# Kernel optimization log

Measured on AMD Instinct MI355X. Metric: run time of the kernel, lower is better.

Reference implementation:

```python
import jax, jax.numpy as jnp
import numpy as np

EPS = 1e-12
N_NODES = 100000
N_EDGES = 1600000
IN_CH = 8
N_CLASSES = 16
MAX_ORDER = 1
N_RINGS = 2


def setup_inputs() -> dict:
    key = jax.random.key(0)
    k0, k1, k2, k3, k4 = jax.random.split(key, 5)
    x = jax.random.normal(k0, (N_NODES, IN_CH), dtype=jnp.float32)
    edge_index = jax.random.randint(k1, (2, N_EDGES), 0, N_NODES)
    precomp = jax.random.normal(k2, (N_EDGES, MAX_ORDER + 1, N_RINGS, 2), dtype=jnp.float32)
    connection = jax.random.normal(k3, (N_EDGES, 2), dtype=jnp.float32)
    # n_orders = (prev_order+1)*(max_order+1) with default prev_order=1 -> 2*(max_order+1)
    n_orders = 2 * (MAX_ORDER + 1)
    radial_profile = jax.random.normal(k4, (n_orders, N_RINGS, N_CLASSES, IN_CH), dtype=jnp.float32) * 0.1
    bias = jnp.zeros((N_CLASSES,), dtype=jnp.float32)
    return dict(x=x, edge_index=edge_index, precomp=precomp,
                connection=connection, radial_profile=radial_profile, bias=bias)


def reference(x, edge_index, precomp, connection, radial_profile, bias):
    # x is stacked with zeros -> complex features with a single stream (M=1, input_order=0).
    # Since input_order==0 only, `connection` (parallel transport) is never applied.
    N = x.shape[0]
    O1 = MAX_ORDER + 1
    src = edge_index[0]  # aggregation targets (flow='target_to_source')
    tgt = edge_index[1]  # gathered neighbours (x_j)
    xjr = x[tgt]                      # [E, F] real part
    xji = jnp.zeros_like(xjr)         # [E, F] imaginary part (zeros by construction)
    # m = |output_order - 0| = output_order; sign = np.sign(m) -> 0 for order 0, +1 otherwise
    signs = jnp.sign(jnp.arange(O1, dtype=x.dtype))
    pre_re = jnp.transpose(precomp[..., 0], (0, 2, 1))          # [E, R, O1]
    pre_im = jnp.transpose(precomp[..., 1], (0, 2, 1)) * signs  # [E, R, O1]
    a_re = xjr[:, None, :, None]      # [E, 1, F, 1]
    a_im = xji[:, None, :, None]
    b_re = pre_re[:, :, None, :]      # [E, R, 1, O1]
    b_im = pre_im[:, :, None, :]
    msg_re = a_re * b_re - a_im * b_im   # [E, R, F, O1]
    msg_im = a_re * b_im + a_im * b_re
    aggr_re = jax.ops.segment_sum(msg_re, src, num_segments=N)  # [N, R, F, O1]
    aggr_im = jax.ops.segment_sum(msg_im, src, num_segments=N)
    # update: m_idx = 0*(max_order+1)+output_order, offset=False
    prof = radial_profile[:O1]        # [O1, R, C, F]
    out_re = jnp.einsum('orcf,nrfo->noc', prof, aggr_re)  # [N, O1, C]
    out_im = jnp.einsum('orcf,nrfo->noc', prof, aggr_im)
    mag = jnp.sqrt(jnp.maximum(out_re * out_re + out_im * out_im, EPS))  # [N, O1, C]
    logits = mag.sum(axis=1) + bias   # [N, C]
    return jax.nn.log_softmax(logits, axis=1)
```

## Files before the change

kernel.cpp:

```cpp
#include <hip/hip_runtime.h>
#include <hip/hip_fp16.h>

#define N_NODES 100000
#define N_EDGES 1600000
#define IN_CH 8
#define N_CLASSES 16

#define NPB 64
#define NPB_SHIFT 6
#define NB ((N_NODES + NPB - 1) / NPB)
#define NB_PAD 1568
#define BIN_T 4096
#define NBLK ((N_EDGES + BIN_T - 1) / BIN_T)
#define MAX_BE 1536

union H2I { __half2 h; int i; };

#define RECBUF_OFF  0
#define BCNT_OFF    ((size_t)N_EDGES * 16)
#define COLSUM_OFF  (BCNT_OFF + (size_t)NBLK * NB_PAD * 4)
#define GBASE_OFF   (COLSUM_OFF + (size_t)NB_PAD * 4)
#define BIN_WS_BYTES (GBASE_OFF + ((size_t)NB + 4) * 4)

#define AGGR_RE_FLOATS (N_NODES * 32)
#define AGGR_IM_FLOATS (N_NODES * 16)
#define WS_FLOATS (AGGR_RE_FLOATS + AGGR_IM_FLOATS)
#define WS_F4 (WS_FLOATS / 4)


__global__ __launch_bounds__(1024) void hist_kernel(const int* __restrict__ ei,
                                                    int* __restrict__ bcnt) {
    __shared__ int h[NB_PAD];
    int t = threadIdx.x;
    for (int i = t; i < NB_PAD; i += 1024) h[i] = 0;
    __syncthreads();
    int base = blockIdx.x * BIN_T;
    int end = base + BIN_T; if (end > N_EDGES) end = N_EDGES;
    for (int e = base + t; e < end; e += 1024)
        atomicAdd(&h[ei[e] >> NPB_SHIFT], 1);
    __syncthreads();
    for (int i = t; i < NB_PAD; i += 1024)
        bcnt[(size_t)blockIdx.x * NB_PAD + i] = h[i];
}

__global__ __launch_bounds__(1024) void colscan_kernel(int* __restrict__ bcnt,
                                                       int* __restrict__ colsum) {
    __shared__ int sbuf[16][65];
    int t = threadIdx.x;
    int r64 = t >> 4, c = t & 15;
    int c0 = blockIdx.x * 16;
    int vals[7];
    int partial = 0;
#pragma unroll
    for (int k = 0; k < 7; ++k) {
        int row = r64 * 7 + k;
        int v = (row < NBLK) ? bcnt[(size_t)row * NB_PAD + c0 + c] : 0;
        vals[k] = v;
        partial += v;
    }
    sbuf[c][r64] = partial;
    __syncthreads();
#pragma unroll
    for (int d = 1; d < 64; d <<= 1) {
        int u = (r64 >= d) ? sbuf[c][r64 - d] : 0;
        __syncthreads();
        sbuf[c][r64] += u;
        __syncthreads();
    }
    int running = sbuf[c][r64] - partial;
#pragma unroll
    for (int k = 0; k < 7; ++k) {
        int row = r64 * 7 + k;
        if (row < NBLK) bcnt[(size_t)row * NB_PAD + c0 + c] = running;
        running += vals[k];
    }
    if (r64 == 63) colsum[c0 + c] = sbuf[c][63];
}

__global__ __launch_bounds__(1024) void base_kernel(const int* __restrict__ colsum,
                                                    int* __restrict__ gbase) {
    __shared__ int buf[1024];
    int t = threadIdx.x;
    int i0 = 2 * t, i1 = 2 * t + 1;
    int v0 = (i0 < NB) ? colsum[i0] : 0;
    int v1 = (i1 < NB) ? colsum[i1] : 0;
    buf[t] = v0 + v1;
    __syncthreads();
#pragma unroll
    for (int d = 1; d < 1024; d <<= 1) {
        int u = (t >= d) ? buf[t - d] : 0;
        __syncthreads();
        buf[t] += u;
        __syncthreads();
    }
    int excl = buf[t] - (v0 + v1);
    if (i0 < NB) gbase[i0] = excl;
    if (i1 < NB) gbase[i1] = excl + v0;
    if (t == 1023) gbase[NB] = buf[1023];
}

__global__ __launch_bounds__(1024) void bin_kernel(
    const int* __restrict__ ei, const float* __restrict__ precomp,
    const int* __restrict__ bcnt, const int* __restrict__ gbase,
    int4* __restrict__ recbuf) {
    __shared__ int lbase[NB];
    __shared__ int lcnt[NB];
    int t = threadIdx.x;
    for (int i = t; i < NB; i += 1024) {
        lbase[i] = gbase[i] + bcnt[(size_t)blockIdx.x * NB_PAD + i];
        lcnt[i] = 0;
    }
    __syncthreads();
    int base = blockIdx.x * BIN_T;
    int end = base + BIN_T; if (end > N_EDGES) end = N_EDGES;
    for (int e = base + t; e < end; e += 1024) {
        int src = ei[e];
        int tgt = ei[N_EDGES + e];
        int b = src >> NPB_SHIFT;
        int rank = atomicAdd(&lcnt[b], 1);
        size_t pos = (size_t)(lbase[b] + rank);
        const float4* pc = (const float4*)(precomp + (size_t)e * 8);
        float4 q0 = pc[0], q1 = pc[1];
        H2I u0, u1, u2;
        u0.h = __floats2half2_rn(q0.x, q0.z);
        u1.h = __floats2half2_rn(q1.x, q1.y);
        u2.h = __floats2half2_rn(q1.z, q1.w);
        int packed = tgt | ((src & (NPB - 1)) << 17);
        recbuf[pos] = make_int4(u0.i, u1.i, u2.i, packed);
    }
}

__global__ __launch_bounds__(512) void aggregate_kernel(
    const int* __restrict__ gbase, const int4* __restrict__ recbuf,
    const float* __restrict__ x,
    const float* __restrict__ prof, const float* __restrict__ bias,
    float* __restrict__ out) {
    __shared__ float sprof[512];
    __shared__ int cnt[NPB];
    __shared__ int start[NPB];
    __shared__ int cur[NPB];
    __shared__ int skey[MAX_BE];
    __shared__ int srec[MAX_BE];
    __shared__ float acc[NPB * 48];

    int t = threadIdx.x, b = blockIdx.x;
    sprof[t] = prof[t];
    if (t < NPB) cnt[t] = 0;
    __syncthreads();

    int lo = gbase[b], hi = gbase[b + 1];
    int n = hi - lo; if (n > MAX_BE) n = MAX_BE;
    const int* ri = (const int*)recbuf;

    for (int k = t; k < n; k += 512) {
        int key = ri[(size_t)(lo + k) * 4 + 3];
        skey[k] = key;
        atomicAdd(&cnt[((unsigned)key) >> 17], 1);
    }
    __syncthreads();

    if (t < 64) {
        int v = cnt[t];
        int s = v;
#pragma unroll
        for (int d = 1; d < 64; d <<= 1) {
            int u = __shfl_up(s, d, 64);
            if (t >= d) s += u;
        }
        start[t] = s - v;
        cur[t] = s - v;
    }
    __syncthreads();

    for (int k = t; k < n; k += 512) {
        int packed = skey[k];
        int nl = ((unsigned)packed) >> 17;
        int p = atomicAdd(&cur[nl], 1);
        srec[p] = (packed & 0x1FFFF) | (k << 17);
    }
    __syncthreads();

    int nl = t >> 3, f = t & 7;
    float a0r0 = 0.f, a1r0 = 0.f, aIr0 = 0.f, a0r1 = 0.f, a1r1 = 0.f, aIr1 = 0.f;
    int s0 = start[nl], n0 = cnt[nl];
    for (int k = 0; k < n0; ++k) {
        int rec = srec[s0 + k];
        int slot = ((unsigned)rec) >> 17;
        int tgt = rec & 0x1FFFF;
        int4 rv = recbuf[(size_t)(lo + slot)];
        H2I u0, u1, u2; u0.i = rv.x; u1.i = rv.y; u2.i = rv.z;
        float2 f0 = __half22float2(u0.h);
        float2 f1 = __half22float2(u1.h);
        float2 f2 = __half22float2(u2.h);
        float xv = x[tgt * IN_CH + f];
        a0r0 = fmaf(xv, f0.x, a0r0);
        a0r1 = fmaf(xv, f0.y, a0r1);
        a1r0 = fmaf(xv, f1.x, a1r0);
        aIr0 = fmaf(xv, f1.y, aIr0);
        a1r1 = fmaf(xv, f2.x, a1r1);
        aIr1 = fmaf(xv, f2.y, aIr1);
    }
    float* a = acc + nl * 48;
    a[f * 3 + 0] = a0r0;  a[f * 3 + 1] = a1r0;  a[f * 3 + 2] = aIr0;
    a[24 + f * 3 + 0] = a0r1;  a[24 + f * 3 + 1] = a1r1;  a[24 + f * 3 + 2] = aIr1;
    __syncthreads();

#pragma unroll
    for (int pass = 0; pass < 2; ++pass) {
        int nl2 = pass * 32 + (t >> 4);
        int c = t & 15;
        int gnode = b * NPB + nl2;
        if (gnode < N_NODES) {
            float re0 = 0.f, re1 = 0.f, im1 = 0.f;
#pragma unroll
            for (int rr = 0; rr < 2; ++rr) {
#pragma unroll
                for (int ff = 0; ff < 8; ++ff) {
                    int idx = nl2 * 48 + rr * 24 + ff * 3;
                    float w0 = sprof[(0 * 2 + rr) * 128 + c * 8 + ff];
                    float w1 = sprof[(1 * 2 + rr) * 128 + c * 8 + ff];
                    re0 = fmaf(w0, acc[idx + 0], re0);
                    re1 = fmaf(w1, acc[idx + 1], re1);
                    im1 = fmaf(w1, acc[idx + 2], im1);
                }
            }
            float mag = sqrtf(fmaxf(re0 * re0, 1e-12f)) +
                        sqrtf(fmaxf(re1 * re1 + im1 * im1, 1e-12f));
            float logit = mag + bias[c];
            float m = logit;
#pragma unroll
            for (int o = 1; o < 16; o <<= 1) m = fmaxf(m, __shfl_xor(m, o, 16));
            float ex = __expf(logit - m);
            float s = ex;
#pragma unroll
            for (int o = 1; o < 16; o <<= 1) s += __shfl_xor(s, o, 16);
            out[gnode * N_CLASSES + c] = (logit - m) - logf(s);
        }
    }
}


__global__ __launch_bounds__(256) void zero_ws_kernel(float4* __restrict__ ws, int n4) {
    int i = blockIdx.x * blockDim.x + threadIdx.x;
    if (i < n4) ws[i] = make_float4(0.f, 0.f, 0.f, 0.f);
}

__global__ __launch_bounds__(256) void edge_kernel(
    const int* __restrict__ ei, const float* __restrict__ x,
    const float* __restrict__ precomp,
    float* __restrict__ aggrRe, float* __restrict__ aggrIm) {
    int gid = blockIdx.x * blockDim.x + threadIdx.x;
    int e = gid >> 3;
    int f = gid & 7;
    if (e >= N_EDGES) return;
    int src = ei[e];
    int tgt = ei[N_EDGES + e];
    float xv = x[tgt * IN_CH + f];
    const float4* pc = (const float4*)(precomp + (size_t)e * 8);
    float4 p0 = pc[0], p1 = pc[1];
    float* ar = aggrRe + (size_t)src * 32;
    atomicAdd(ar + ((0 * 8 + f) * 2 + 0), xv * p0.x);
    atomicAdd(ar + ((1 * 8 + f) * 2 + 0), xv * p0.z);
    atomicAdd(ar + ((0 * 8 + f) * 2 + 1), xv * p1.x);
    atomicAdd(ar + ((1 * 8 + f) * 2 + 1), xv * p1.z);
    float* ai = aggrIm + (size_t)src * 16;
    atomicAdd(ai + (0 * 8 + f), xv * p1.y);
    atomicAdd(ai + (1 * 8 + f), xv * p1.w);
}

__global__ __launch_bounds__(256) void node_kernel(
    const float* __restrict__ aggrRe, const float* __restrict__ aggrIm,
    const float* __restrict__ prof, const float* __restrict__ bias,
    float* __restrict__ out) {
    __shared__ float sprof[512];
    for (int i = threadIdx.x; i < 512; i += blockDim.x) sprof[i] = prof[i];
    __syncthreads();
    int gid = blockIdx.x * blockDim.x + threadIdx.x;
    int n = gid >> 4;
    int c = gid & 15;
    if (n >= N_NODES) return;
    const float* ar = aggrRe + (size_t)n * 32;
    const float* ai = aggrIm + (size_t)n * 16;
    float re0 = 0.f, re1 = 0.f, im1 = 0.f;
#pragma unroll
    for (int r = 0; r < 2; ++r)
#pragma unroll
        for (int f = 0; f < 8; ++f) {
            float a0 = ar[(r * 8 + f) * 2 + 0];
            float a1 = ar[(r * 8 + f) * 2 + 1];
            float aI = ai[r * 8 + f];
            float w0 = sprof[(0 * 2 + r) * 128 + c * 8 + f];
            float w1 = sprof[(1 * 2 + r) * 128 + c * 8 + f];
            re0 = fmaf(w0, a0, re0);
            re1 = fmaf(w1, a1, re1);
            im1 = fmaf(w1, aI, im1);
        }
    float mag = sqrtf(fmaxf(re0 * re0, 1e-12f)) +
                sqrtf(fmaxf(re1 * re1 + im1 * im1, 1e-12f));
    float logit = mag + bias[c];
    float m = logit;
#pragma unroll
    for (int o = 1; o < 16; o <<= 1) m = fmaxf(m, __shfl_xor(m, o, 16));
    float ex = __expf(logit - m);
    float s = ex;
#pragma unroll
    for (int o = 1; o < 16; o <<= 1) s += __shfl_xor(s, o, 16);
    out[n * N_CLASSES + c] = (logit - m) - logf(s);
}


extern "C" void kernel_launch(void* const* d_in, const int* in_sizes, int n_in,
                              void* d_out, int out_size, void* d_ws, size_t ws_size,
                              hipStream_t stream) {
    const float* x       = (const float*)d_in[0];
    const int*   ei      = (const int*)d_in[1];
    const float* precomp = (const float*)d_in[2];
    const float* prof    = (const float*)d_in[4];
    const float* bias    = (const float*)d_in[5];
    float* out = (float*)d_out;

    if (ws_size >= BIN_WS_BYTES) {
        char* ws = (char*)d_ws;
        int4* recbuf = (int4*)(ws + RECBUF_OFF);
        int* bcnt    = (int*)(ws + BCNT_OFF);
        int* colsum  = (int*)(ws + COLSUM_OFF);
        int* gbase   = (int*)(ws + GBASE_OFF);

        hist_kernel<<<NBLK, 1024, 0, stream>>>(ei, bcnt);
        colscan_kernel<<<NB_PAD / 16, 1024, 0, stream>>>(bcnt, colsum);
        base_kernel<<<1, 1024, 0, stream>>>(colsum, gbase);
        bin_kernel<<<NBLK, 1024, 0, stream>>>(ei, precomp, bcnt, gbase, recbuf);
        aggregate_kernel<<<NB, 512, 0, stream>>>(gbase, recbuf, x, prof, bias, out);
    } else {
        float* aggrRe = (float*)d_ws;
        float* aggrIm = aggrRe + AGGR_RE_FLOATS;
        zero_ws_kernel<<<(WS_F4 + 255) / 256, 256, 0, stream>>>((float4*)d_ws, WS_F4);
        int edge_threads = N_EDGES * 8;
        edge_kernel<<<(edge_threads + 255) / 256, 256, 0, stream>>>(ei, x, precomp, aggrRe, aggrIm);
        int node_threads = N_NODES * 16;
        node_kernel<<<(node_threads + 255) / 256, 256, 0, stream>>>(aggrRe, aggrIm, prof, bias, out);
    }
}
```

Before: 74.47 us.

## Locally sort edges by bucket in shared memory before scattering records

The binning kernel now histograms each tile's edges by destination bucket in shared memory, scans the counts, and writes a bucket-sorted permutation of edge indices to shared memory. Threads then walk the sorted order, so consecutive threads write to consecutive recbuf slots inside the same bucket, making the scattered 16-byte stores more coalesced. The cost is an extra pass over the edge sources, a 1024-wide block scan with many barriers, and gathered rather than sequential reads of precomp and edge indices.

```diff
diff --git a/kernel.cpp b/kernel.cpp
--- a/kernel.cpp
+++ b/kernel.cpp
@@ -104,21 +104,60 @@
     const int* __restrict__ bcnt, const int* __restrict__ gbase,
     int4* __restrict__ recbuf) {
     __shared__ int lbase[NB];
-    __shared__ int lcnt[NB];
+    __shared__ int cnt[NB];
+    __shared__ int tstart[NB];
+    __shared__ unsigned short sei[BIN_T];
+    __shared__ int sscan[1024];
+
     int t = threadIdx.x;
+    int base = blockIdx.x * BIN_T;
+    int tn = N_EDGES - base; if (tn > BIN_T) tn = BIN_T;
+
     for (int i = t; i < NB; i += 1024) {
         lbase[i] = gbase[i] + bcnt[(size_t)blockIdx.x * NB_PAD + i];
-        lcnt[i] = 0;
-    }
-    __syncthreads();
-    int base = blockIdx.x * BIN_T;
-    int end = base + BIN_T; if (end > N_EDGES) end = N_EDGES;
-    for (int e = base + t; e < end; e += 1024) {
+        cnt[i] = 0;
+    }
+    __syncthreads();
+
+    for (int k = t; k < tn; k += 1024)
+        atomicAdd(&cnt[ei[base + k] >> NPB_SHIFT], 1);
+    __syncthreads();
+
+    {
+        int i0 = 2 * t, i1 = 2 * t + 1;
+        int v0 = (i0 < NB) ? cnt[i0] : 0;
+        int v1 = (i1 < NB) ? cnt[i1] : 0;
+        sscan[t] = v0 + v1;
+        __syncthreads();
+#pragma unroll
+        for (int d = 1; d < 1024; d <<= 1) {
+            int u = (t >= d) ? sscan[t - d] : 0;
+            __syncthreads();
+            sscan[t] += u;
+            __syncthreads();
+        }
+        int excl = sscan[t] - (v0 + v1);
+        if (i0 < NB) tstart[i0] = excl;
+        if (i1 < NB) tstart[i1] = excl + v0;
+    }
+    __syncthreads();
+    for (int i = t; i < NB; i += 1024) cnt[i] = tstart[i];
+    __syncthreads();
+
+    for (int k = t; k < tn; k += 1024) {
+        int b = ei[base + k] >> NPB_SHIFT;
+        int s = atomicAdd(&cnt[b], 1);
+        sei[s] = (unsigned short)k;
+    }
+    __syncthreads();
+
+    for (int s = t; s < tn; s += 1024) {
+        int k = (int)sei[s];
+        int e = base + k;
         int src = ei[e];
         int tgt = ei[N_EDGES + e];
         int b = src >> NPB_SHIFT;
-        int rank = atomicAdd(&lcnt[b], 1);
-        size_t pos = (size_t)(lbase[b] + rank);
+        int pos = lbase[b] + (s - tstart[b]);
         const float4* pc = (const float4*)(precomp + (size_t)e * 8);
         float4 q0 = pc[0], q1 = pc[1];
         H2I u0, u1, u2;
@@ -126,7 +165,7 @@
         u1.h = __floats2half2_rn(q1.x, q1.y);
         u2.h = __floats2half2_rn(q1.z, q1.w);
         int packed = tgt | ((src & (NPB - 1)) << 17);
-        recbuf[pos] = make_int4(u0.i, u1.i, u2.i, packed);
+        recbuf[(size_t)pos] = make_int4(u0.i, u1.i, u2.i, packed);
     }
 }
 
```

After: 89.54 us. +20.2%, slower.
